# Optimization experiments

Hardware: AMD Instinct MI355X
Metric: run time of the kernel (lower is better)

## Reference

```python
import jax, jax.numpy as jnp
import numpy as np
import math

B, S, D, H, FF, L, V = 4, 2048, 512, 8, 2048, 4, 256
WINDOW, STRIDE, NGLOBAL = 256, 128, 16  # sparse pattern: causal & (local | strided | global)


def setup_inputs() -> dict:
    key = jax.random.key(0)
    ks = jax.random.split(key, 12)
    g = lambda k, shp: jax.random.normal(k, shp, dtype=jnp.float32) * 0.02
    return {
        "src_tokens": jax.random.randint(ks[0], (B, S), 0, V, dtype=jnp.int32),
        "emb": g(ks[1], (V, D)),
        "b_out": jnp.zeros((V,), jnp.float32),
        "Wq": g(ks[2], (L, D, D)), "bq": jnp.zeros((L, D), jnp.float32),
        "Wk": g(ks[3], (L, D, D)), "bk": jnp.zeros((L, D), jnp.float32),
        "Wv": g(ks[4], (L, D, D)), "bv": jnp.zeros((L, D), jnp.float32),
        "Wo": g(ks[5], (L, D, D)), "bo": jnp.zeros((L, D), jnp.float32),
        "ln1_g": jnp.ones((L, D), jnp.float32), "ln1_b": jnp.zeros((L, D), jnp.float32),
        "W1": g(ks[6], (L, D, FF)), "b1": jnp.zeros((L, FF), jnp.float32),
        "W2": g(ks[7], (L, FF, D)), "b2": jnp.zeros((L, D), jnp.float32),
        "ln2_g": jnp.ones((L, D), jnp.float32), "ln2_b": jnp.zeros((L, D), jnp.float32),
    }


def _pos_enc(seq_len, d_model):
    pos = jnp.arange(seq_len, dtype=jnp.float32)[:, None]
    div = jnp.exp(jnp.arange(0, d_model, 2, dtype=jnp.float32) * (-math.log(10000.0) / d_model))
    pe = jnp.zeros((seq_len, d_model), jnp.float32)
    pe = pe.at[:, 0::2].set(jnp.sin(pos * div)).at[:, 1::2].set(jnp.cos(pos * div))
    return pe


def _ln(x, g, b):
    m = x.mean(-1, keepdims=True)
    v = ((x - m) ** 2).mean(-1, keepdims=True)
    return (x - m) * jax.lax.rsqrt(v + 1e-5) * g + b


def _sparse_mask(seq_len):
    i = jnp.arange(seq_len)[:, None]
    j = jnp.arange(seq_len)[None, :]
    causal = j <= i
    local = (i - j) < WINDOW
    strided = ((i - j) % STRIDE) == 0
    glob = j < NGLOBAL
    return causal & (local | strided | glob)  # [S, S] bool


def reference(src_tokens, emb, b_out, Wq, bq, Wk, bk, Wv, bv, Wo, bo,
              ln1_g, ln1_b, W1, b1, W2, b2, ln2_g, ln2_b):
    dh = D // H
    x = emb[src_tokens] * math.sqrt(D) + _pos_enc(S, D)  # [B,S,D] (dropout inactive at eval)
    mask = _sparse_mask(S)
    for l in range(L):
        q = (x @ Wq[l] + bq[l]).reshape(B, S, H, dh)
        k = (x @ Wk[l] + bk[l]).reshape(B, S, H, dh)
        v = (x @ Wv[l] + bv[l]).reshape(B, S, H, dh)
        scores = jnp.einsum('bihd,bjhd->bhij', q, k) / math.sqrt(dh)
        scores = jnp.where(mask, scores, jnp.float32(-1e9))
        attn = jax.nn.softmax(scores, axis=-1)
        o = jnp.einsum('bhij,bjhd->bihd', attn, v).reshape(B, S, D)
        x = _ln(x + o @ Wo[l] + bo[l], ln1_g[l], ln1_b[l])      # post-LN residual
        h = jax.nn.relu(x @ W1[l] + b1[l])
        x = _ln(x + h @ W2[l] + b2[l], ln2_g[l], ln2_b[l])
    return x @ emb.T + b_out  # tied output projection -> [B,S,V]
```

## Files before the change

### kernel.cpp

```cpp
#include <hip/hip_runtime.h>
#include <hip/hip_bf16.h>
#include <math.h>

#define B_  4
#define S_  2048
#define D_  512
#define H_  8
#define DH_ 64
#define FF_ 2048
#define L_  4
#define V_  256
#define NTOK (B_ * S_)
#define XN  ((size_t)NTOK * D_)

typedef __attribute__((ext_vector_type(8))) short bf16x8;
typedef __attribute__((ext_vector_type(4))) float f32x4;
typedef __attribute__((ext_vector_type(8))) unsigned short u16x8;
typedef __attribute__((ext_vector_type(4))) unsigned short u16x4;

typedef const __attribute__((address_space(1))) unsigned int* gptr_u32;
typedef __attribute__((address_space(3))) unsigned int* lptr_u32;

__device__ __forceinline__ float bf2f(unsigned short u) {
    return __uint_as_float((unsigned)u << 16);
}
__device__ __forceinline__ unsigned short f2bf_bits(float f) {
    __hip_bfloat16 t = __float2bfloat16(f);
    return *(unsigned short*)&t;
}

__global__ void pe_table_kernel(float* __restrict__ PE) {
    int s = blockIdx.x;
    int d = threadIdx.x * 2;
    float ang = (float)s * expf((float)d * (-logf(10000.0f) / (float)D_));
    PE[(size_t)s * D_ + d]     = sinf(ang);
    PE[(size_t)s * D_ + d + 1] = cosf(ang);
}

__global__ void embed_kernel(const int* __restrict__ tok,
                             const float* __restrict__ emb,
                             const float* __restrict__ PE,
                             float* __restrict__ X,
                             __hip_bfloat16* __restrict__ Xb) {
    int bs = blockIdx.x;
    int s = bs % S_;
    int t = tok[bs];
    const float scale = 22.62741699796952f;
    int d = threadIdx.x * 4;
    float4 e = *(const float4*)(emb + (size_t)t * D_ + d);
    float4 p = *(const float4*)(PE + (size_t)s * D_ + d);
    float4 v = make_float4(e.x * scale + p.x, e.y * scale + p.y,
                           e.z * scale + p.z, e.w * scale + p.w);
    *(float4*)(X + (size_t)bs * D_ + d) = v;
    u16x4 pk = { f2bf_bits(v.x), f2bf_bits(v.y), f2bf_bits(v.z), f2bf_bits(v.w) };
    *(u16x4*)((unsigned short*)Xb + (size_t)bs * D_ + d) = pk;
}

__global__ void transpose_conv_kernel(const float* __restrict__ W,
                                      __hip_bfloat16* __restrict__ Wt,
                                      int K, int N) {
    const float* Wl = W + (size_t)blockIdx.z * K * N;
    __hip_bfloat16* Wtl = Wt + (size_t)blockIdx.z * K * N;
    __shared__ float t[32][33];
    int k0 = blockIdx.y * 32, n0 = blockIdx.x * 32;
    int tx = threadIdx.x & 31, ty = threadIdx.x >> 5;
    #pragma unroll
    for (int q = 0; q < 4; ++q)
        t[ty + q * 8][tx] = Wl[(size_t)(k0 + ty + q * 8) * N + n0 + tx];
    __syncthreads();
    #pragma unroll
    for (int q = 0; q < 4; ++q)
        Wtl[(size_t)(n0 + ty + q * 8) * K + k0 + tx] =
            __float2bfloat16(t[tx][ty + q * 8]);
}

__global__ void transpose_qkv_kernel(const float* __restrict__ Wq,
                                     const float* __restrict__ Wk,
                                     const float* __restrict__ Wv,
                                     __hip_bfloat16* __restrict__ dst) {
    int z = blockIdx.z, l = z / 3, which = z % 3;
    const float* src = (which == 0 ? Wq : which == 1 ? Wk : Wv) + (size_t)l * D_ * D_;
    __hip_bfloat16* d = dst + (size_t)l * 1536 * D_ + (size_t)which * D_ * D_;
    __shared__ float t[32][33];
    int k0 = blockIdx.y * 32, n0 = blockIdx.x * 32;
    int tx = threadIdx.x & 31, ty = threadIdx.x >> 5;
    #pragma unroll
    for (int q = 0; q < 4; ++q)
        t[ty + q * 8][tx] = src[(size_t)(k0 + ty + q * 8) * D_ + n0 + tx];
    __syncthreads();
    #pragma unroll
    for (int q = 0; q < 4; ++q)
        d[(size_t)(n0 + ty + q * 8) * D_ + k0 + tx] =
            __float2bfloat16(t[tx][ty + q * 8]);
}

__global__ void conv_bf16_kernel(const float* __restrict__ in,
                                 __hip_bfloat16* __restrict__ out, int n) {
    int i = blockIdx.x * 256 + threadIdx.x;
    if (i < n) out[i] = __float2bfloat16(in[i]);
}

template <int BM, int RELU, int OUT_MODE>
__global__ __launch_bounds__(256)
void gemm_bf16_kernel(const __hip_bfloat16* __restrict__ A,
                      const __hip_bfloat16* __restrict__ Bt,
                      const float* __restrict__ bias0,
                      const float* __restrict__ bias1,
                      const float* __restrict__ bias2,
                      float* __restrict__ Cf,
                      __hip_bfloat16* __restrict__ Cb0,
                      __hip_bfloat16* __restrict__ Cb1,
                      __hip_bfloat16* __restrict__ Cb2,
                      __hip_bfloat16* __restrict__ CbT,
                      int M, int N, int K, int lda) {
    constexpr int MI = BM / 32;
    __shared__ unsigned short SMEM[2 * BM * 32 + 2 * 128 * 32];
    unsigned short* As0 = SMEM;
    unsigned short* Bs0 = SMEM + 2 * BM * 32;
    int tid = threadIdx.x;
    int lane = tid & 63, wid = tid >> 6;
    int wm = (wid >> 1) * (BM / 2), wn = (wid & 1) * 64;
    int g = lane >> 4, il = lane & 15;

    int gx = gridDim.x;
    int fid = blockIdx.x + gx * blockIdx.y;
    int cpx = (gx * gridDim.y) >> 3;
    int swz = (fid & 7) * cpx + (fid >> 3);
    int m0 = (swz / gx) * BM, n0 = (swz % gx) * 128;

    size_t koff = 0;
    if constexpr (OUT_MODE == 5) koff = (size_t)blockIdx.z * K;

    auto stage = [&](int buf, int k0) {
        #pragma unroll
        for (int q = 0; q < BM / 64; ++q) {
            int idx = q * 256 + tid;
            int r = idx >> 2, c = idx & 3;
            int csw = (c ^ r) & 3;
            const __hip_bfloat16* sa = A + (size_t)(m0 + r) * lda + koff + k0 + csw * 8;
            __builtin_amdgcn_global_load_lds((gptr_u32)(const void*)sa,
                                             (lptr_u32)(void*)&As0[buf * BM * 32 + idx * 8], 16, 0, 0);
        }
        #pragma unroll
        for (int q = 0; q < 2; ++q) {
            int idx = q * 256 + tid;
            int r = idx >> 2, c = idx & 3;
            int csw = (c ^ r) & 3;
            const __hip_bfloat16* sb = Bt + (size_t)(n0 + r) * lda + koff + k0 + csw * 8;
            __builtin_amdgcn_global_load_lds((gptr_u32)(const void*)sb,
                                             (lptr_u32)(void*)&Bs0[buf * 128 * 32 + idx * 8], 16, 0, 0);
        }
    };

    f32x4 acc[MI][4] = {};
    int NT = K >> 5;
    stage(0, 0);

    for (int t = 0; t < NT; ++t) {
        int cur = t & 1;
        if (t + 1 < NT) {
            stage(cur ^ 1, (t + 1) << 5);
            if constexpr (BM == 128)
                asm volatile("s_waitcnt vmcnt(4)" ::: "memory");
            else
                asm volatile("s_waitcnt vmcnt(3)" ::: "memory");
        } else {
            asm volatile("s_waitcnt vmcnt(0)" ::: "memory");
        }
        __builtin_amdgcn_s_barrier();

        bf16x8 af[MI], bf[4];
        #pragma unroll
        for (int i = 0; i < MI; ++i) {
            int m = wm + i * 16 + il;
            af[i] = *(const bf16x8*)&As0[cur * BM * 32 + m * 32 + ((g ^ m) & 3) * 8];
        }
        #pragma unroll
        for (int j = 0; j < 4; ++j) {
            int n = wn + j * 16 + il;
            bf[j] = *(const bf16x8*)&Bs0[cur * 128 * 32 + n * 32 + ((g ^ n) & 3) * 8];
        }
        #pragma unroll
        for (int i = 0; i < MI; ++i)
            #pragma unroll
            for (int j = 0; j < 4; ++j)
                acc[i][j] = __builtin_amdgcn_mfma_f32_16x16x32_bf16(
                    af[i], bf[j], acc[i][j], 0, 0, 0);

        __builtin_amdgcn_s_barrier();
    }

    if constexpr (OUT_MODE == 0) {
        #pragma unroll
        for (int j = 0; j < 4; ++j) {
            int col = n0 + wn + j * 16 + il;
            float bv = bias0[col];
            #pragma unroll
            for (int i = 0; i < MI; ++i) {
                #pragma unroll
                for (int r = 0; r < 4; ++r) {
                    int row = m0 + wm + i * 16 + g * 4 + r;
                    Cf[(size_t)row * N + col] = acc[i][j][r] + bv;
                }
            }
        }
    } else {
        int seg = 0, nseg = 0;
        const float* bias = bias0;
        if constexpr (OUT_MODE == 4) {
            seg = n0 >> 9;
            bias = seg == 0 ? bias0 : seg == 1 ? bias1 : bias2;
            nseg = n0 & 511;
        }
        unsigned short* Ct = SMEM;
        #pragma unroll
        for (int j = 0; j < 4; ++j) {
            int colt = wn + j * 16 + il;
            float bv;
            if constexpr (OUT_MODE == 4)      bv = bias[nseg + colt];
            else if constexpr (OUT_MODE == 5) bv = blockIdx.z ? 0.0f : bias0[n0 + colt];
            else                              bv = bias0[n0 + colt];
            #pragma unroll
            for (int i = 0; i < MI; ++i) {
                int rowt = wm + i * 16 + g * 4;
                #pragma unroll
                for (int r = 0; r < 4; ++r) {
                    float v = acc[i][j][r] + bv;
                    if (RELU) v = fmaxf(v, 0.0f);
                    Ct[(rowt + r) * 128 + colt] = f2bf_bits(v);
                }
            }
        }
        __syncthreads();

        if constexpr (OUT_MODE == 4) {
            __hip_bfloat16* Crow = seg == 0 ? Cb0 : seg == 1 ? Cb1 : Cb2;
            #pragma unroll
            for (int q = 0; q < BM / 16; ++q) {
                int idx = q * 256 + tid;
                int row = idx >> 4, ch = idx & 15;
                *(u16x8*)((unsigned short*)Crow + (size_t)(m0 + row) * 512 + nseg + ch * 8) =
                    *(const u16x8*)&Ct[row * 128 + ch * 8];
            }
            if (seg == 2) {
                int bb = m0 >> 11, s0base = m0 & 2047;
                #pragma unroll
                for (int q = 0; q < BM / 16; ++q) {
                    int idx = q * 256 + tid;
                    int colt = idx / (BM / 8);
                    int sc   = idx % (BM / 8);
                    int coll = nseg + colt, hh = coll >> 6, dh = coll & 63;
                    u16x8 pk;
                    #pragma unroll
                    for (int e = 0; e < 8; ++e) pk[e] = Ct[(sc * 8 + e) * 128 + colt];
                    *(u16x8*)((unsigned short*)CbT +
                              ((size_t)((bb * 8 + hh) * 64 + dh) * 2048) + s0base + sc * 8) = pk;
                }
            }
        } else {
            __hip_bfloat16* Cd;
            if constexpr (OUT_MODE == 5) Cd = blockIdx.z ? Cb1 : Cb0;
            else                         Cd = Cb0;
            #pragma unroll
            for (int q = 0; q < BM / 16; ++q) {
                int idx = q * 256 + tid;
                int row = idx >> 4, ch = idx & 15;
                *(u16x8*)((unsigned short*)Cd + (size_t)(m0 + row) * N + n0 + ch * 8) =
                    *(const u16x8*)&Ct[row * 128 + ch * 8];
            }
        }
    }
}

__device__ __forceinline__ bf16x8 lds_frag(const unsigned short* base, int row, int chunk) {
    int byte = (row << 7) + (((chunk ^ (row & 7)) & 7) << 4);
    return *(const bf16x8*)((const char*)base + byte);
}

__global__ __launch_bounds__(256)
void attn_mfma_kernel(const __hip_bfloat16* __restrict__ Q,
                      const __hip_bfloat16* __restrict__ K,
                      const __hip_bfloat16* __restrict__ V,
                      const __hip_bfloat16* __restrict__ VT,
                      __hip_bfloat16* __restrict__ O) {
    __shared__ unsigned short SM[4096 + 4096 + 4096];
    unsigned short* Ks = SM;
    unsigned short* Vs = SM + 4096;

    int d = blockIdx.x + 32 * (blockIdx.y + 8 * blockIdx.z);
    int xcd = d & 7;
    int rest = d >> 3;
    int gsub = rest & 3;
    int qt = 31 - (rest >> 2);
    int grp = xcd * 4 + gsub;
    int h = grp & 7, b = grp >> 3;
    int i0 = qt * 64;

    int tid = threadIdx.x, lane = tid & 63, wv = tid >> 6;
    int g = lane >> 4, il = lane & 15, g4 = g * 4;

    int nloc = min(i0 >> 6, 4) + 1;
    int add0 = (i0 > 256);
    int nt = nloc + add0;

    const size_t vt_off = (size_t)((b * 8 + h) * 64) * 2048;
    auto j0_of = [&](int t) { return (t < nloc) ? (i0 - 64 * t) : 0; };

    auto stage = [&](int j0) {
        #pragma unroll
        for (int q = 0; q < 2; ++q) {
            int idx = q * 256 + tid;
            int row = idx >> 3, c = idx & 7;
            int csw = c ^ (row & 7);
            const __hip_bfloat16* sk = K + (size_t)(b * 2048 + j0 + row) * 512 + h * 64 + csw * 8;
            __builtin_amdgcn_global_load_lds((gptr_u32)(const void*)sk,
                                             (lptr_u32)(void*)&Ks[idx * 8], 16, 0, 0);
            const __hip_bfloat16* sv = VT + vt_off + (size_t)row * 2048 + j0 + csw * 8;
            __builtin_amdgcn_global_load_lds((gptr_u32)(const void*)sv,
                                             (lptr_u32)(void*)&Vs[idx * 8], 16, 0, 0);
        }
    };

    int iq = i0 + wv * 16 + il;
    bf16x8 qf[2];
    #pragma unroll
    for (int kh = 0; kh < 2; ++kh)
        qf[kh] = *(const bf16x8*)(Q + (size_t)(b * 2048 + iq) * 512 + h * 64 + kh * 32 + g * 8);

    stage(j0_of(0));

    float qfl[16];
    #pragma unroll
    for (int kh = 0; kh < 2; ++kh)
        #pragma unroll
        for (int e = 0; e < 8; ++e)
            qfl[kh * 8 + e] = bf2f(((u16x8)qf[kh])[e]);

    unsigned short* myP = SM + 8192 + wv * 1024;
    f32x4 o[4] = {};
    float os[16] = {};
    float m = -1e30f, l = 0.0f;
    const float CSC = 0.18033688011112042f;

    const unsigned short* Kbase = (const unsigned short*)(K + (size_t)b * 2048 * 512 + h * 64);
    const unsigned short* Vbase = (const unsigned short*)(V + (size_t)b * 2048 * 512 + h * 64);
    for (int j = iq - 384; j >= 16; j -= 128) {
        const unsigned short* kr = Kbase + (size_t)j * 512;
        u16x8 k0 = *(const u16x8*)(kr + g * 8);
        u16x8 k1 = *(const u16x8*)(kr + 32 + g * 8);
        float dot = 0.0f;
        #pragma unroll
        for (int e = 0; e < 8; ++e)
            dot += qfl[e] * bf2f(k0[e]) + qfl[8 + e] * bf2f(k1[e]);
        dot += __shfl_xor(dot, 16);
        dot += __shfl_xor(dot, 32);
        float s2 = dot * CSC;
        float mn = fmaxf(m, s2);
        float al = exp2f(m - mn);
        float p = exp2f(s2 - mn);
        l = l * al + p;
        m = mn;
        const unsigned short* vr = Vbase + (size_t)j * 512;
        u16x8 v0 = *(const u16x8*)(vr + g * 8);
        u16x8 v1 = *(const u16x8*)(vr + 32 + g * 8);
        #pragma unroll
        for (int e = 0; e < 8; ++e) {
            os[e]     = os[e]     * al + p * bf2f(v0[e]);
            os[8 + e] = os[8 + e] * al + p * bf2f(v1[e]);
        }
    }

    for (int t = 0; t < nt; ++t) {
        asm volatile("s_waitcnt vmcnt(0)" ::: "memory");
        __builtin_amdgcn_s_barrier();
        int j0 = j0_of(t);
        bool gtile = (t >= nloc);
        bool dtile = (t == 0);

        f32x4 s[4] = {};
        __builtin_amdgcn_s_setprio(1);
        if (gtile) {
            #pragma unroll
            for (int kh = 0; kh < 2; ++kh) {
                bf16x8 a = lds_frag(Ks, il, kh * 4 + g);
                s[0] = __builtin_amdgcn_mfma_f32_16x16x32_bf16(a, qf[kh], s[0], 0, 0, 0);
            }
        } else if (dtile) {
            #pragma unroll
            for (int kh = 0; kh < 2; ++kh)
                #pragma unroll
                for (int jn = 0; jn < 4; ++jn)
                    if (jn <= wv) {
                        bf16x8 a = lds_frag(Ks, jn * 16 + il, kh * 4 + g);
                        s[jn] = __builtin_amdgcn_mfma_f32_16x16x32_bf16(a, qf[kh], s[jn], 0, 0, 0);
                    }
        } else {
            #pragma unroll
            for (int kh = 0; kh < 2; ++kh)
                #pragma unroll
                for (int jn = 0; jn < 4; ++jn) {
                    bf16x8 a = lds_frag(Ks, jn * 16 + il, kh * 4 + g);
                    s[jn] = __builtin_amdgcn_mfma_f32_16x16x32_bf16(a, qf[kh], s[jn], 0, 0, 0);
                }
        }
        __builtin_amdgcn_s_setprio(0);

        float mloc = -1e30f;
        if (gtile) {
            #pragma unroll
            for (int r = 0; r < 4; ++r) {
                float sv = s[0][r] * CSC;
                s[0][r] = sv;
                mloc = fmaxf(mloc, sv);
            }
        } else if (dtile) {
            #pragma unroll
            for (int jn = 0; jn < 4; ++jn) {
                if (jn < wv) {
                    #pragma unroll
                    for (int r = 0; r < 4; ++r) {
                        float sv = s[jn][r] * CSC;
                        s[jn][r] = sv;
                        mloc = fmaxf(mloc, sv);
                    }
                } else if (jn == wv) {
                    #pragma unroll
                    for (int r = 0; r < 4; ++r) {
                        float sv = (g4 + r <= il) ? s[jn][r] * CSC : -1e30f;
                        s[jn][r] = sv;
                        mloc = fmaxf(mloc, sv);
                    }
                }
            }
        } else if (t == 4) {
            #pragma unroll
            for (int jn = 0; jn < 4; ++jn)
                #pragma unroll
                for (int r = 0; r < 4; ++r) {
                    int jg = j0 + jn * 16 + g4 + r;
                    int dij = iq - jg;
                    bool ok = (dij < 256) || ((dij & 127) == 0) || (jg < 16);
                    float sv = ok ? s[jn][r] * CSC : -1e30f;
                    s[jn][r] = sv;
                    mloc = fmaxf(mloc, sv);
                }
        } else {
            #pragma unroll
            for (int jn = 0; jn < 4; ++jn)
                #pragma unroll
                for (int r = 0; r < 4; ++r) {
                    float sv = s[jn][r] * CSC;
                    s[jn][r] = sv;
                    mloc = fmaxf(mloc, sv);
                }
        }
        mloc = fmaxf(mloc, __shfl_xor(mloc, 16));
        mloc = fmaxf(mloc, __shfl_xor(mloc, 32));
        float mn = fmaxf(m, mloc);
        float al = exp2f(m - mn);

        float lloc = 0.0f;
        if (gtile) {
            #pragma unroll
            for (int r = 0; r < 4; ++r) {
                float p = exp2f(s[0][r] - mn);
                s[0][r] = p;
                lloc += p;
            }
        } else {
            #pragma unroll
            for (int jn = 0; jn < 4; ++jn) {
                if (dtile && jn > wv) continue;
                #pragma unroll
                for (int r = 0; r < 4; ++r) {
                    float p = exp2f(s[jn][r] - mn);
                    s[jn][r] = p;
                    lloc += p;
                }
            }
        }
        lloc += __shfl_xor(lloc, 16);
        lloc += __shfl_xor(lloc, 32);
        l = l * al + lloc;
        m = mn;

        if (!__all(al == 1.0f)) {
            float ar[4];
            #pragma unroll
            for (int r = 0; r < 4; ++r) ar[r] = __shfl(al, g4 + r);
            #pragma unroll
            for (int dn = 0; dn < 4; ++dn)
                #pragma unroll
                for (int r = 0; r < 4; ++r) o[dn][r] *= ar[r];
            #pragma unroll
            for (int e = 0; e < 16; ++e) os[e] *= al;
        }

        #pragma unroll
        for (int jn = 0; jn < 4; ++jn) {
            if (gtile && jn >= 2) continue;
            u16x4 pk = { 0, 0, 0, 0 };
            bool live = gtile ? (jn == 0) : (!dtile || jn <= wv);
            if (live) {
                #pragma unroll
                for (int r = 0; r < 4; ++r) pk[r] = f2bf_bits(s[jn][r]);
            }
            int byte = ((il << 7) + (jn << 5) + (g << 3)) ^ ((il & 7) << 4);
            *(u16x4*)((char*)myP + byte) = pk;
        }
        int khmax = (gtile || (dtile && wv < 2)) ? 1 : 2;
        __builtin_amdgcn_s_setprio(1);
        #pragma unroll
        for (int kh = 0; kh < 2; ++kh) {
            if (kh < khmax) {
                bf16x8 pa = lds_frag(myP, il, kh * 4 + g);
                #pragma unroll
                for (int dn = 0; dn < 4; ++dn) {
                    bf16x8 bv = lds_frag(Vs, dn * 16 + il, kh * 4 + g);
                    o[dn] = __builtin_amdgcn_mfma_f32_16x16x32_bf16(pa, bv, o[dn], 0, 0, 0);
                }
            }
        }
        __builtin_amdgcn_s_setprio(0);

        __builtin_amdgcn_s_barrier();
        if (t + 1 < nt) stage(j0_of(t + 1));
    }

    float* osl = (float*)SM + wv * 1024;
    #pragma unroll
    for (int kh = 0; kh < 2; ++kh)
        #pragma unroll
        for (int e = 0; e < 8; ++e)
            osl[il * 64 + kh * 32 + g * 8 + e] = os[kh * 8 + e];
    __syncthreads();

    float li[4];
    #pragma unroll
    for (int r = 0; r < 4; ++r) li[r] = 1.0f / __shfl(l, g4 + r);
    #pragma unroll
    for (int dn = 0; dn < 4; ++dn)
        #pragma unroll
        for (int r = 0; r < 4; ++r) {
            int row = i0 + wv * 16 + g4 + r;
            float add = osl[(g4 + r) * 64 + dn * 16 + il];
            O[(size_t)(b * 2048 + row) * 512 + h * 64 + dn * 16 + il] =
                __float2bfloat16((o[dn][r] + add) * li[r]);
        }
}

__global__ __launch_bounds__(256)
void add_ln_kernel(float* __restrict__ X,
                   const __hip_bfloat16* __restrict__ T1,
                   const __hip_bfloat16* __restrict__ T2,
                   const float* __restrict__ g,
                   const float* __restrict__ bb,
                   __hip_bfloat16* __restrict__ Xb) {
    size_t row = blockIdx.x * 4 + (threadIdx.x >> 6);
    int lane = threadIdx.x & 63;
    int d0 = lane * 8;
    float4 x0 = *(const float4*)(X + row * D_ + d0);
    float4 x1 = *(const float4*)(X + row * D_ + d0 + 4);
    u16x8 t1 = *(const u16x8*)((const unsigned short*)T1 + row * D_ + d0);
    u16x8 t2 = *(const u16x8*)((const unsigned short*)T2 + row * D_ + d0);
    float v[8] = { x0.x + bf2f(t1[0]) + bf2f(t2[0]), x0.y + bf2f(t1[1]) + bf2f(t2[1]),
                   x0.z + bf2f(t1[2]) + bf2f(t2[2]), x0.w + bf2f(t1[3]) + bf2f(t2[3]),
                   x1.x + bf2f(t1[4]) + bf2f(t2[4]), x1.y + bf2f(t1[5]) + bf2f(t2[5]),
                   x1.z + bf2f(t1[6]) + bf2f(t2[6]), x1.w + bf2f(t1[7]) + bf2f(t2[7]) };
    float sum = 0.0f;
    #pragma unroll
    for (int q = 0; q < 8; ++q) sum += v[q];
    #pragma unroll
    for (int o = 32; o; o >>= 1) sum += __shfl_xor(sum, o);
    float mean = sum * (1.0f / D_);
    float var = 0.0f;
    #pragma unroll
    for (int q = 0; q < 8; ++q) { float dd = v[q] - mean; var += dd * dd; }
    #pragma unroll
    for (int o = 32; o; o >>= 1) var += __shfl_xor(var, o);
    var *= (1.0f / D_);
    float r = rsqrtf(var + 1e-5f);
    float4 g0 = *(const float4*)(g + d0),  g1 = *(const float4*)(g + d0 + 4);
    float4 b0 = *(const float4*)(bb + d0), b1 = *(const float4*)(bb + d0 + 4);
    float y[8];
    y[0] = (v[0]-mean)*r*g0.x+b0.x; y[1] = (v[1]-mean)*r*g0.y+b0.y;
    y[2] = (v[2]-mean)*r*g0.z+b0.z; y[3] = (v[3]-mean)*r*g0.w+b0.w;
    y[4] = (v[4]-mean)*r*g1.x+b1.x; y[5] = (v[5]-mean)*r*g1.y+b1.y;
    y[6] = (v[6]-mean)*r*g1.z+b1.z; y[7] = (v[7]-mean)*r*g1.w+b1.w;
    *(float4*)(X + row * D_ + d0)     = make_float4(y[0], y[1], y[2], y[3]);
    *(float4*)(X + row * D_ + d0 + 4) = make_float4(y[4], y[5], y[6], y[7]);
    u16x8 pk;
    #pragma unroll
    for (int q = 0; q < 8; ++q) pk[q] = f2bf_bits(y[q]);
    *(u16x8*)((unsigned short*)Xb + row * D_ + d0) = pk;
}

extern "C" void kernel_launch(void* const* d_in, const int* in_sizes, int n_in,
                              void* d_out, int out_size, void* d_ws, size_t ws_size,
                              hipStream_t stream) {
    const int*   tok   = (const int*)  d_in[0];
    const float* emb   = (const float*)d_in[1];
    const float* b_out = (const float*)d_in[2];
    const float* Wq    = (const float*)d_in[3];
    const float* bq    = (const float*)d_in[4];
    const float* Wk    = (const float*)d_in[5];
    const float* bk    = (const float*)d_in[6];
    const float* Wv    = (const float*)d_in[7];
    const float* bv    = (const float*)d_in[8];
    const float* Wo    = (const float*)d_in[9];
    const float* bo    = (const float*)d_in[10];
    const float* ln1g  = (const float*)d_in[11];
    const float* ln1b  = (const float*)d_in[12];
    const float* W1    = (const float*)d_in[13];
    const float* b1    = (const float*)d_in[14];
    const float* W2    = (const float*)d_in[15];
    const float* b2    = (const float*)d_in[16];
    const float* ln2g  = (const float*)d_in[17];
    const float* ln2b  = (const float*)d_in[18];
    float* out = (float*)d_out;

    char* w = (char*)d_ws;
    auto alloc = [&](size_t bytes) {
        char* p = w;
        w += (bytes + 255) & ~(size_t)255;
        return p;
    };
    float*          X   = (float*)         alloc(XN * 4);
    __hip_bfloat16* Xb  = (__hip_bfloat16*)alloc(XN * 2);
    __hip_bfloat16* Tb  = (__hip_bfloat16*)alloc(XN * 2);
    char* uni = alloc(XN * 2 * 5);
    __hip_bfloat16* Qb  = (__hip_bfloat16*)uni;
    __hip_bfloat16* Kb  = Qb + XN;
    __hip_bfloat16* Vb  = Kb + XN;
    __hip_bfloat16* VTb = Vb + XN;
    __hip_bfloat16* Ob  = VTb + XN;
    __hip_bfloat16* Hb  = (__hip_bfloat16*)uni;
    __hip_bfloat16* T2wo = Qb;
    __hip_bfloat16* T2w2 = Ob;
    __hip_bfloat16* Wqkvt = (__hip_bfloat16*)alloc((size_t)L_ * 1536 * D_ * 2);
    __hip_bfloat16* Wot  = (__hip_bfloat16*)alloc((size_t)L_ * D_ * D_ * 2);
    __hip_bfloat16* W1t  = (__hip_bfloat16*)alloc((size_t)L_ * D_ * FF_ * 2);
    __hip_bfloat16* W2t  = (__hip_bfloat16*)alloc((size_t)L_ * FF_ * D_ * 2);
    __hip_bfloat16* embb = (__hip_bfloat16*)alloc((size_t)V_ * D_ * 2);
    float*          PE   = (float*)alloc((size_t)S_ * D_ * 4);

    {
        pe_table_kernel<<<S_, 256, 0, stream>>>(PE);
        dim3 gqkv(D_ / 32, D_ / 32, L_ * 3);
        transpose_qkv_kernel<<<gqkv, 256, 0, stream>>>(Wq, Wk, Wv, Wqkvt);
        dim3 gdd(D_ / 32, D_ / 32, L_);
        transpose_conv_kernel<<<gdd, 256, 0, stream>>>(Wo, Wot, D_, D_);
        dim3 g1(FF_ / 32, D_ / 32, L_);
        transpose_conv_kernel<<<g1, 256, 0, stream>>>(W1, W1t, D_, FF_);
        dim3 g2(D_ / 32, FF_ / 32, L_);
        transpose_conv_kernel<<<g2, 256, 0, stream>>>(W2, W2t, FF_, D_);
        conv_bf16_kernel<<<(V_ * D_ + 255) / 256, 256, 0, stream>>>(emb, embb, V_ * D_);
    }

    embed_kernel<<<NTOK, 128, 0, stream>>>(tok, emb, PE, X, Xb);

    dim3 blk(256);
    dim3 gqkv(1536 / 128, NTOK / 128);
    dim3 gsplit(D_ / 128, NTOK / 64, 2);
    dim3 gff (FF_ / 128, NTOK / 128);
    dim3 gout(V_ / 128, NTOK / 64);
    dim3 gattn(S_ / 64, H_, B_);
    dim3 gln(NTOK / 4);

    for (int l = 0; l < L_; ++l) {
        const __hip_bfloat16* wqkv = Wqkvt + (size_t)l * 1536 * D_;
        const __hip_bfloat16* wot = Wot + (size_t)l * D_ * D_;
        const __hip_bfloat16* w1t = W1t + (size_t)l * D_ * FF_;
        const __hip_bfloat16* w2t = W2t + (size_t)l * FF_ * D_;

        gemm_bf16_kernel<128, 0, 4><<<gqkv, blk, 0, stream>>>(
            Xb, wqkv, bq + l * D_, bk + l * D_, bv + l * D_,
            nullptr, Qb, Kb, Vb, VTb, NTOK, 1536, D_, D_);

        attn_mfma_kernel<<<gattn, blk, 0, stream>>>(Qb, Kb, Vb, VTb, Ob);

        gemm_bf16_kernel<64, 0, 5><<<gsplit, blk, 0, stream>>>(
            Ob, wot, bo + l * D_, nullptr, nullptr,
            nullptr, Tb, T2wo, nullptr, nullptr, NTOK, D_, 256, D_);
        add_ln_kernel<<<gln, blk, 0, stream>>>(X, Tb, T2wo, ln1g + l * D_, ln1b + l * D_, Xb);

        gemm_bf16_kernel<128, 1, 1><<<gff, blk, 0, stream>>>(
            Xb, w1t, b1 + l * FF_, nullptr, nullptr,
            nullptr, Hb, nullptr, nullptr, nullptr, NTOK, FF_, D_, D_);

        gemm_bf16_kernel<64, 0, 5><<<gsplit, blk, 0, stream>>>(
            Hb, w2t, b2 + l * D_, nullptr, nullptr,
            nullptr, Tb, T2w2, nullptr, nullptr, NTOK, D_, 1024, FF_);
        add_ln_kernel<<<gln, blk, 0, stream>>>(X, Tb, T2w2, ln2g + l * D_, ln2b + l * D_, Xb);
    }

    gemm_bf16_kernel<64, 0, 0><<<gout, blk, 0, stream>>>(
        Xb, embb, b_out, nullptr, nullptr,
        out, nullptr, nullptr, nullptr, nullptr, NTOK, V_, D_, D_);
}
```

Baseline: 674.0 us.

## Enlarge attention query tile to 128 rows with 8 waves sharing staged K/V

```diff
diff --git a/kernel.cpp b/kernel.cpp
--- a/kernel.cpp
+++ b/kernel.cpp
@@ -277,48 +277,44 @@
     return *(const bf16x8*)((const char*)base + byte);
 }
 
-__global__ __launch_bounds__(256)
+__global__ __launch_bounds__(512)
 void attn_mfma_kernel(const __hip_bfloat16* __restrict__ Q,
                       const __hip_bfloat16* __restrict__ K,
                       const __hip_bfloat16* __restrict__ V,
                       const __hip_bfloat16* __restrict__ VT,
                       __hip_bfloat16* __restrict__ O) {
-    __shared__ unsigned short SM[4096 + 4096 + 4096];
+    __shared__ unsigned short SM[4096 + 4096 + 8192];
     unsigned short* Ks = SM;
     unsigned short* Vs = SM + 4096;
 
-    int d = blockIdx.x + 32 * (blockIdx.y + 8 * blockIdx.z);
+    int d = blockIdx.x + 16 * (blockIdx.y + 8 * blockIdx.z);
     int xcd = d & 7;
     int rest = d >> 3;
     int gsub = rest & 3;
-    int qt = 31 - (rest >> 2);
+    int qtB = 15 - (rest >> 2);
     int grp = xcd * 4 + gsub;
     int h = grp & 7, b = grp >> 3;
-    int i0 = qt * 64;
+    int i0 = qtB * 128;
 
     int tid = threadIdx.x, lane = tid & 63, wv = tid >> 6;
     int g = lane >> 4, il = lane & 15, g4 = g * 4;
 
-    int nloc = min(i0 >> 6, 4) + 1;
-    int add0 = (i0 > 256);
-    int nt = nloc + add0;
+    int nlist = min((i0 >> 6) + 2, 7);
+    int nt = nlist + (i0 >= 384 ? 1 : 0);
 
     const size_t vt_off = (size_t)((b * 8 + h) * 64) * 2048;
-    auto j0_of = [&](int t) { return (t < nloc) ? (i0 - 64 * t) : 0; };
+    auto j0_of = [&](int t) { return (t < nlist) ? (i0 + 64 - 64 * t) : 0; };
 
     auto stage = [&](int j0) {
-        #pragma unroll
-        for (int q = 0; q < 2; ++q) {
-            int idx = q * 256 + tid;
-            int row = idx >> 3, c = idx & 7;
-            int csw = c ^ (row & 7);
-            const __hip_bfloat16* sk = K + (size_t)(b * 2048 + j0 + row) * 512 + h * 64 + csw * 8;
-            __builtin_amdgcn_global_load_lds((gptr_u32)(const void*)sk,
-                                             (lptr_u32)(void*)&Ks[idx * 8], 16, 0, 0);
-            const __hip_bfloat16* sv = VT + vt_off + (size_t)row * 2048 + j0 + csw * 8;
-            __builtin_amdgcn_global_load_lds((gptr_u32)(const void*)sv,
-                                             (lptr_u32)(void*)&Vs[idx * 8], 16, 0, 0);
-        }
+        int idx = tid;
+        int row = idx >> 3, c = idx & 7;
+        int csw = c ^ (row & 7);
+        const __hip_bfloat16* sk = K + (size_t)(b * 2048 + j0 + row) * 512 + h * 64 + csw * 8;
+        __builtin_amdgcn_global_load_lds((gptr_u32)(const void*)sk,
+                                         (lptr_u32)(void*)&Ks[idx * 8], 16, 0, 0);
+        const __hip_bfloat16* sv = VT + vt_off + (size_t)row * 2048 + j0 + csw * 8;
+        __builtin_amdgcn_global_load_lds((gptr_u32)(const void*)sv,
+                                         (lptr_u32)(void*)&Vs[idx * 8], 16, 0, 0);
     };
 
     int iq = i0 + wv * 16 + il;
@@ -344,7 +340,8 @@
 
     const unsigned short* Kbase = (const unsigned short*)(K + (size_t)b * 2048 * 512 + h * 64);
     const unsigned short* Vbase = (const unsigned short*)(V + (size_t)b * 2048 * 512 + h * 64);
-    for (int j = iq - 384; j >= 16; j -= 128) {
+    int js = iq - 384 - ((wv >= 4) ? 128 : 0);
+    for (int j = js; j >= 16; j -= 128) {
         const unsigned short* kr = Kbase + (size_t)j * 512;
         u16x8 k0 = *(const u16x8*)(kr + g * 8);
         u16x8 k1 = *(const u16x8*)(kr + 32 + g * 8);
@@ -374,159 +371,124 @@
         asm volatile("s_waitcnt vmcnt(0)" ::: "memory");
         __builtin_amdgcn_s_barrier();
         int j0 = j0_of(t);
-        bool gtile = (t >= nloc);
-        bool dtile = (t == 0);
-
-        f32x4 s[4] = {};
-        __builtin_amdgcn_s_setprio(1);
-        if (gtile) {
-            #pragma unroll
-            for (int kh = 0; kh < 2; ++kh) {
-                bf16x8 a = lds_frag(Ks, il, kh * 4 + g);
-                s[0] = __builtin_amdgcn_mfma_f32_16x16x32_bf16(a, qf[kh], s[0], 0, 0, 0);
-            }
-        } else if (dtile) {
-            #pragma unroll
-            for (int kh = 0; kh < 2; ++kh)
-                #pragma unroll
-                for (int jn = 0; jn < 4; ++jn)
-                    if (jn <= wv) {
+        bool gtile = (t >= nlist);
+        bool wdead = (!gtile) && (j0 > i0 + wv * 16 + 15);
+
+        if (!wdead) {
+            f32x4 s[4] = {};
+            __builtin_amdgcn_s_setprio(1);
+            if (gtile) {
+                #pragma unroll
+                for (int kh = 0; kh < 2; ++kh) {
+                    bf16x8 a = lds_frag(Ks, il, kh * 4 + g);
+                    s[0] = __builtin_amdgcn_mfma_f32_16x16x32_bf16(a, qf[kh], s[0], 0, 0, 0);
+                }
+            } else {
+                #pragma unroll
+                for (int kh = 0; kh < 2; ++kh)
+                    #pragma unroll
+                    for (int jn = 0; jn < 4; ++jn) {
                         bf16x8 a = lds_frag(Ks, jn * 16 + il, kh * 4 + g);
                         s[jn] = __builtin_amdgcn_mfma_f32_16x16x32_bf16(a, qf[kh], s[jn], 0, 0, 0);
                     }
-        } else {
-            #pragma unroll
-            for (int kh = 0; kh < 2; ++kh)
-                #pragma unroll
-                for (int jn = 0; jn < 4; ++jn) {
-                    bf16x8 a = lds_frag(Ks, jn * 16 + il, kh * 4 + g);
-                    s[jn] = __builtin_amdgcn_mfma_f32_16x16x32_bf16(a, qf[kh], s[jn], 0, 0, 0);
-                }
-        }
-        __builtin_amdgcn_s_setprio(0);
-
-        float mloc = -1e30f;
-        if (gtile) {
-            #pragma unroll
-            for (int r = 0; r < 4; ++r) {
-                float sv = s[0][r] * CSC;
-                s[0][r] = sv;
-                mloc = fmaxf(mloc, sv);
-            }
-        } else if (dtile) {
-            #pragma unroll
-            for (int jn = 0; jn < 4; ++jn) {
-                if (jn < wv) {
+            }
+            __builtin_amdgcn_s_setprio(0);
+
+            float mloc = -1e30f;
+            if (gtile) {
+                #pragma unroll
+                for (int r = 0; r < 4; ++r) {
+                    float sv = s[0][r] * CSC;
+                    s[0][r] = sv;
+                    mloc = fmaxf(mloc, sv);
+                }
+            } else {
+                #pragma unroll
+                for (int jn = 0; jn < 4; ++jn)
                     #pragma unroll
                     for (int r = 0; r < 4; ++r) {
-                        float sv = s[jn][r] * CSC;
+                        int jg = j0 + jn * 16 + g4 + r;
+                        int dij = iq - jg;
+                        bool ok = (dij >= 0) &&
+                                  ((dij < 256) || ((dij & 127) == 0) || (jg < 16));
+                        float sv = ok ? s[jn][r] * CSC : -1e30f;
                         s[jn][r] = sv;
                         mloc = fmaxf(mloc, sv);
                     }
-                } else if (jn == wv) {
+            }
+            mloc = fmaxf(mloc, __shfl_xor(mloc, 16));
+            mloc = fmaxf(mloc, __shfl_xor(mloc, 32));
+            float mn = fmaxf(m, mloc);
+            float al = exp2f(m - mn);
+
+            float lloc = 0.0f;
+            if (gtile) {
+                #pragma unroll
+                for (int r = 0; r < 4; ++r) {
+                    float p = exp2f(s[0][r] - mn);
+                    s[0][r] = p;
+                    lloc += p;
+                }
+            } else {
+                #pragma unroll
+                for (int jn = 0; jn < 4; ++jn)
                     #pragma unroll
                     for (int r = 0; r < 4; ++r) {
-                        float sv = (g4 + r <= il) ? s[jn][r] * CSC : -1e30f;
-                        s[jn][r] = sv;
-                        mloc = fmaxf(mloc, sv);
+                        float p = exp2f(s[jn][r] - mn);
+                        s[jn][r] = p;
+                        lloc += p;
                     }
-                }
-            }
-        } else if (t == 4) {
-            #pragma unroll
-            for (int jn = 0; jn < 4; ++jn)
-                #pragma unroll
-                for (int r = 0; r < 4; ++r) {
-                    int jg = j0 + jn * 16 + g4 + r;
-                    int dij = iq - jg;
-                    bool ok = (dij < 256) || ((dij & 127) == 0) || (jg < 16);
-                    float sv = ok ? s[jn][r] * CSC : -1e30f;
-                    s[jn][r] = sv;
-                    mloc = fmaxf(mloc, sv);
-                }
-        } else {
-            #pragma unroll
-            for (int jn = 0; jn < 4; ++jn)
-                #pragma unroll
-                for (int r = 0; r < 4; ++r) {
-                    float sv = s[jn][r] * CSC;
-                    s[jn][r] = sv;
-                    mloc = fmaxf(mloc, sv);
-                }
-        }
-        mloc = fmaxf(mloc, __shfl_xor(mloc, 16));
-        mloc = fmaxf(mloc, __shfl_xor(mloc, 32));
-        float mn = fmaxf(m, mloc);
-        float al = exp2f(m - mn);
-
-        float lloc = 0.0f;
-        if (gtile) {
-            #pragma unroll
-            for (int r = 0; r < 4; ++r) {
-                float p = exp2f(s[0][r] - mn);
-                s[0][r] = p;
-                lloc += p;
-            }
-        } else {
+            }
+            lloc += __shfl_xor(lloc, 16);
+            lloc += __shfl_xor(lloc, 32);
+            l = l * al + lloc;
+            m = mn;
+
+            if (!__all(al == 1.0f)) {
+                float ar[4];
+                #pragma unroll
+                for (int r = 0; r < 4; ++r) ar[r] = __shfl(al, g4 + r);
+                #pragma unroll
+                for (int dn = 0; dn < 4; ++dn)
+                    #pragma unroll
+                    for (int r = 0; r < 4; ++r) o[dn][r] *= ar[r];
+                #pragma unroll
+                for (int e = 0; e < 16; ++e) os[e] *= al;
+            }
+
             #pragma unroll
             for (int jn = 0; jn < 4; ++jn) {
-                if (dtile && jn > wv) continue;
-                #pragma unroll
-                for (int r = 0; r < 4; ++r) {
-                    float p = exp2f(s[jn][r] - mn);
-                    s[jn][r] = p;
-                    lloc += p;
-                }
-            }
-        }
-        lloc += __shfl_xor(lloc, 16);
-        lloc += __shfl_xor(lloc, 32);
-        l = l * al + lloc;
-        m = mn;
-
-        if (!__all(al == 1.0f)) {
-            float ar[4];
+                if (gtile && jn >= 2) continue;
+                u16x4 pk = { 0, 0, 0, 0 };
+                bool live = gtile ? (jn == 0) : true;
+                if (live) {
+                    #pragma unroll
+                    for (int r = 0; r < 4; ++r) pk[r] = f2bf_bits(s[jn][r]);
+                }
+                int byte = ((il << 7) + (jn << 5) + (g << 3)) ^ ((il & 7) << 4);
+                *(u16x4*)((char*)myP + byte) = pk;
+            }
+            int khmax = gtile ? 1 : 2;
+            __builtin_amdgcn_s_setprio(1);
             #pragma unroll
-            for (int r = 0; r < 4; ++r) ar[r] = __shfl(al, g4 + r);
-            #pragma unroll
-            for (int dn = 0; dn < 4; ++dn)
-                #pragma unroll
-                for (int r = 0; r < 4; ++r) o[dn][r] *= ar[r];
-            #pragma unroll
-            for (int e = 0; e < 16; ++e) os[e] *= al;
-        }
-
-        #pragma unroll
-        for (int jn = 0; jn < 4; ++jn) {
-            if (gtile && jn >= 2) continue;
-            u16x4 pk = { 0, 0, 0, 0 };
-            bool live = gtile ? (jn == 0) : (!dtile || jn <= wv);
-            if (live) {
-                #pragma unroll
-                for (int r = 0; r < 4; ++r) pk[r] = f2bf_bits(s[jn][r]);
-            }
-            int byte = ((il << 7) + (jn << 5) + (g << 3)) ^ ((il & 7) << 4);
-            *(u16x4*)((char*)myP + byte) = pk;
-        }
-        int khmax = (gtile || (dtile && wv < 2)) ? 1 : 2;
-        __builtin_amdgcn_s_setprio(1);
-        #pragma unroll
-        for (int kh = 0; kh < 2; ++kh) {
-            if (kh < khmax) {
-                bf16x8 pa = lds_frag(myP, il, kh * 4 + g);
-                #pragma unroll
-                for (int dn = 0; dn < 4; ++dn) {
-                    bf16x8 bv = lds_frag(Vs, dn * 16 + il, kh * 4 + g);
-                    o[dn] = __builtin_amdgcn_mfma_f32_16x16x32_bf16(pa, bv, o[dn], 0, 0, 0);
-                }
-            }
-        }
-        __builtin_amdgcn_s_setprio(0);
+            for (int kh = 0; kh < 2; ++kh) {
+                if (kh < khmax) {
+                    bf16x8 pa = lds_frag(myP, il, kh * 4 + g);
+                    #pragma unroll
+                    for (int dn = 0; dn < 4; ++dn) {
+                        bf16x8 bv = lds_frag(Vs, dn * 16 + il, kh * 4 + g);
+                        o[dn] = __builtin_amdgcn_mfma_f32_16x16x32_bf16(pa, bv, o[dn], 0, 0, 0);
+                    }
+                }
+            }
+            __builtin_amdgcn_s_setprio(0);
+        }
 
         __builtin_amdgcn_s_barrier();
         if (t + 1 < nt) stage(j0_of(t + 1));
     }
 
+    __syncthreads();
     float* osl = (float*)SM + wv * 1024;
     #pragma unroll
     for (int kh = 0; kh < 2; ++kh)
@@ -660,11 +622,12 @@
     embed_kernel<<<NTOK, 128, 0, stream>>>(tok, emb, PE, X, Xb);
 
     dim3 blk(256);
+    dim3 blk512(512);
     dim3 gqkv(1536 / 128, NTOK / 128);
     dim3 gsplit(D_ / 128, NTOK / 64, 2);
     dim3 gff (FF_ / 128, NTOK / 128);
     dim3 gout(V_ / 128, NTOK / 64);
-    dim3 gattn(S_ / 64, H_, B_);
+    dim3 gattn(S_ / 128, H_, B_);
     dim3 gln(NTOK / 4);
 
     for (int l = 0; l < L_; ++l) {
@@ -677,7 +640,7 @@
             Xb, wqkv, bq + l * D_, bk + l * D_, bv + l * D_,
             nullptr, Qb, Kb, Vb, VTb, NTOK, 1536, D_, D_);
 
-        attn_mfma_kernel<<<gattn, blk, 0, stream>>>(Qb, Kb, Vb, VTb, Ob);
+        attn_mfma_kernel<<<gattn, blk512, 0, stream>>>(Qb, Kb, Vb, VTb, Ob);
 
         gemm_bf16_kernel<64, 0, 5><<<gsplit, blk, 0, stream>>>(
             Ob, wot, bo + l * D_, nullptr, nullptr,
```

Measured after the change: 678.3 us. Within noise of the previous version (+0.6%).
